# Performance work log

Hardware: AMD Instinct MI355X
Metric: run time of the kernel (lower is better)

The kernel has to match this reference:

```python
import jax, jax.numpy as jnp
import numpy as np
from jax import lax

NBINS = 256


def setup_inputs() -> dict:
    key = jax.random.key(0)
    y_pred = jax.random.uniform(key, (64, 3, 512, 512), dtype=jnp.float32)
    return {"y_pred": y_pred}


def reference(y_pred):
    # Faithful to: per-batch torch.histc(bins=256) (range = data min/max),
    # normalize to probs, entropy in bits with 0*log2(0)=0, mean over batch.
    B = y_pred.shape[0]
    x = y_pred.reshape(B, -1)  # [B, N]
    mn = jnp.min(x, axis=1, keepdims=True)
    mx = jnp.max(x, axis=1, keepdims=True)
    # torch.histc: if min == max they are adjusted to min-1 / max+1
    rng = jnp.where(mx > mn, mx - mn, 2.0)
    lo = jnp.where(mx > mn, mn, mn - 1.0)
    idx = jnp.clip(((x - lo) * (NBINS / rng)).astype(jnp.int32), 0, NBINS - 1)
    idx = lax.stop_gradient(idx)  # binning is non-differentiable (as in torch.histc)
    hist = jax.vmap(lambda i: jnp.bincount(i, length=NBINS))(idx)  # [B, 256]
    hist = hist.astype(y_pred.dtype)
    p = hist / jnp.sum(hist, axis=1, keepdims=True)
    safe_p = jnp.where(p == 0, 1.0, p)  # log2(1)=0 -> contributes 0
    ent = -jnp.sum(p * jnp.log2(safe_p), axis=1)  # [B], entropy in bits
    return jnp.mean(ent)
```

## Files before the change

kernel.cpp:

```cpp
#include <hip/hip_runtime.h>

#define NBINS   256
#define B       64
#define NPB     786432
#define NF4     (NPB / 4)
#define BPB     16
#define THREADS 256

__device__ __forceinline__ unsigned fenc(float f) {
    unsigned u = __float_as_uint(f);
    return (u & 0x80000000u) ? ~u : (u | 0x80000000u);
}
__device__ __forceinline__ float fdec(unsigned u) {
    unsigned v = (u & 0x80000000u) ? (u & 0x7FFFFFFFu) : ~u;
    return __uint_as_float(v);
}

__global__ __launch_bounds__(THREADS) void k_init(unsigned* __restrict__ mm,
                                                  unsigned* __restrict__ hist) {
    int i = blockIdx.x * blockDim.x + threadIdx.x;
    if (i < B) { mm[2 * i] = 0xFFFFFFFFu; mm[2 * i + 1] = 0u; }
    if (i < B * NBINS) hist[i] = 0u;
}

__global__ __launch_bounds__(THREADS) void k_minmax(const float4* __restrict__ x,
                                                    unsigned* __restrict__ mm) {
    const int batch = blockIdx.x / BPB;
    const int blk   = blockIdx.x % BPB;
    const float4* p = x + (long long)batch * NF4;

    float mn = 3.402823466e38f, mx = -3.402823466e38f;
    int t = blk * THREADS + threadIdx.x;
    #pragma unroll 4
    for (int i = t; i < NF4; i += BPB * THREADS) {
        float4 v = p[i];
        mn = fminf(mn, fminf(fminf(v.x, v.y), fminf(v.z, v.w)));
        mx = fmaxf(mx, fmaxf(fmaxf(v.x, v.y), fmaxf(v.z, v.w)));
    }
    for (int o = 32; o > 0; o >>= 1) {
        mn = fminf(mn, __shfl_down(mn, o));
        mx = fmaxf(mx, __shfl_down(mx, o));
    }
    __shared__ float smn[4], smx[4];
    int wid = threadIdx.x >> 6;
    if ((threadIdx.x & 63) == 0) { smn[wid] = mn; smx[wid] = mx; }
    __syncthreads();
    if (threadIdx.x == 0) {
        mn = fminf(fminf(smn[0], smn[1]), fminf(smn[2], smn[3]));
        mx = fmaxf(fmaxf(smx[0], smx[1]), fmaxf(smx[2], smx[3]));
        atomicMin(&mm[2 * batch],     fenc(mn));
        atomicMax(&mm[2 * batch + 1], fenc(mx));
    }
}

__global__ __launch_bounds__(THREADS) void k_hist(const float4* __restrict__ x,
                                                  const unsigned* __restrict__ mm,
                                                  unsigned* __restrict__ hist) {
    const int batch = blockIdx.x / BPB;
    const int blk   = blockIdx.x % BPB;

    __shared__ unsigned lh[4][NBINS];
    for (int i = threadIdx.x; i < 4 * NBINS; i += THREADS)
        ((unsigned*)lh)[i] = 0u;
    __syncthreads();

    const float mn = fdec(mm[2 * batch]);
    const float mx = fdec(mm[2 * batch + 1]);
    const float rng   = (mx > mn) ? (mx - mn) : 2.0f;
    const float lo    = (mx > mn) ? mn : (mn - 1.0f);
    const float scale = (float)NBINS / rng;

    unsigned* h = lh[threadIdx.x >> 6];
    const float4* p = x + (long long)batch * NF4;
    int t = blk * THREADS + threadIdx.x;
    for (int i = t; i < NF4; i += BPB * THREADS) {
        float4 v = p[i];
        int i0 = (int)((v.x - lo) * scale);
        int i1 = (int)((v.y - lo) * scale);
        int i2 = (int)((v.z - lo) * scale);
        int i3 = (int)((v.w - lo) * scale);
        i0 = min(max(i0, 0), NBINS - 1);
        i1 = min(max(i1, 0), NBINS - 1);
        i2 = min(max(i2, 0), NBINS - 1);
        i3 = min(max(i3, 0), NBINS - 1);
        atomicAdd(&h[i0], 1u);
        atomicAdd(&h[i1], 1u);
        atomicAdd(&h[i2], 1u);
        atomicAdd(&h[i3], 1u);
    }
    __syncthreads();

    unsigned* gh = hist + batch * NBINS;
    for (int i = threadIdx.x; i < NBINS; i += THREADS) {
        unsigned s = lh[0][i] + lh[1][i] + lh[2][i] + lh[3][i];
        if (s) atomicAdd(&gh[i], s);
    }
}

__global__ __launch_bounds__(THREADS) void k_entropy(const unsigned* __restrict__ hist,
                                                     float* __restrict__ out) {
    const float invN = 1.0f / (float)NPB;
    float sum = 0.0f;
    for (int b = 0; b < B; ++b) {
        unsigned c = hist[b * NBINS + threadIdx.x];
        if (c) {
            float pv = (float)c * invN;
            sum += pv * log2f(pv);
        }
    }
    for (int o = 32; o > 0; o >>= 1) sum += __shfl_down(sum, o);
    __shared__ float s[4];
    int wid = threadIdx.x >> 6;
    if ((threadIdx.x & 63) == 0) s[wid] = sum;
    __syncthreads();
    if (threadIdx.x == 0)
        out[0] = -(s[0] + s[1] + s[2] + s[3]) / (float)B;
}

extern "C" void kernel_launch(void* const* d_in, const int* in_sizes, int n_in,
                              void* d_out, int out_size, void* d_ws, size_t ws_size,
                              hipStream_t stream) {
    const float* x = (const float*)d_in[0];
    float* out = (float*)d_out;
    unsigned* mm   = (unsigned*)d_ws;
    unsigned* hist = mm + 2 * B;

    hipLaunchKernelGGL(k_init, dim3((B * NBINS + THREADS - 1) / THREADS),
                       dim3(THREADS), 0, stream, mm, hist);
    hipLaunchKernelGGL(k_minmax, dim3(B * BPB), dim3(THREADS), 0, stream,
                       (const float4*)x, mm);
    hipLaunchKernelGGL(k_hist, dim3(B * BPB), dim3(THREADS), 0, stream,
                       (const float4*)x, mm, hist);
    hipLaunchKernelGGL(k_entropy, dim3(1), dim3(THREADS), 0, stream, hist, out);
}
```

Baseline: 302.0 us.

## Fuse min/max, histogram and entropy into one cooperative kernel with grid syncs

Merges the init, min/max, histogram and entropy kernels into a single cooperative launch that uses grid-wide syncs between phases. Each block writes its own partial min/max, and the histogram phase reduces the 16 per-batch partials directly, which removes the encoded float atomics and the separate init kernel. The histogram zeroing is folded into the min/max phase. This saves launch gaps and keeps data possibly warm in cache between passes. It adds grid-sync cost and depends on all 1024 blocks being co-resident, with a fallback to three separate kernels if the cooperative launch fails.

```diff
diff --git a/kernel.cpp b/kernel.cpp
--- a/kernel.cpp
+++ b/kernel.cpp
@@ -1,4 +1,7 @@
 #include <hip/hip_runtime.h>
+#include <hip/hip_cooperative_groups.h>
+
+namespace cg = cooperative_groups;
 
 #define NBINS   256
 #define B       64
@@ -6,28 +9,17 @@
 #define NF4     (NPB / 4)
 #define BPB     16
 #define THREADS 256
+#define GRID    (B * BPB)
 
-__device__ __forceinline__ unsigned fenc(float f) {
-    unsigned u = __float_as_uint(f);
-    return (u & 0x80000000u) ? ~u : (u | 0x80000000u);
-}
-__device__ __forceinline__ float fdec(unsigned u) {
-    unsigned v = (u & 0x80000000u) ? (u & 0x7FFFFFFFu) : ~u;
-    return __uint_as_float(v);
-}
 
-__global__ __launch_bounds__(THREADS) void k_init(unsigned* __restrict__ mm,
-                                                  unsigned* __restrict__ hist) {
-    int i = blockIdx.x * blockDim.x + threadIdx.x;
-    if (i < B) { mm[2 * i] = 0xFFFFFFFFu; mm[2 * i + 1] = 0u; }
-    if (i < B * NBINS) hist[i] = 0u;
-}
+__device__ __forceinline__ void phase_minmax(const float4* __restrict__ x,
+                                             float2* __restrict__ pb,
+                                             unsigned* __restrict__ bhist) {
+    if (blockIdx.x < B) bhist[blockIdx.x * NBINS + threadIdx.x] = 0u;
 
-__global__ __launch_bounds__(THREADS) void k_minmax(const float4* __restrict__ x,
-                                                    unsigned* __restrict__ mm) {
     const int batch = blockIdx.x / BPB;
     const int blk   = blockIdx.x % BPB;
-    const float4* p = x + (long long)batch * NF4;
+    const float4* p = x + (size_t)batch * NF4;
 
     float mn = 3.402823466e38f, mx = -3.402823466e38f;
     int t = blk * THREADS + threadIdx.x;
@@ -48,30 +40,34 @@
     if (threadIdx.x == 0) {
         mn = fminf(fminf(smn[0], smn[1]), fminf(smn[2], smn[3]));
         mx = fmaxf(fmaxf(smx[0], smx[1]), fmaxf(smx[2], smx[3]));
-        atomicMin(&mm[2 * batch],     fenc(mn));
-        atomicMax(&mm[2 * batch + 1], fenc(mx));
+        pb[blockIdx.x] = make_float2(mn, mx);
     }
 }
 
-__global__ __launch_bounds__(THREADS) void k_hist(const float4* __restrict__ x,
-                                                  const unsigned* __restrict__ mm,
-                                                  unsigned* __restrict__ hist) {
+__device__ __forceinline__ void phase_hist(const float4* __restrict__ x,
+                                           const float2* __restrict__ pb,
+                                           unsigned* __restrict__ bhist) {
     const int batch = blockIdx.x / BPB;
     const int blk   = blockIdx.x % BPB;
+
+    float mn = 3.402823466e38f, mx = -3.402823466e38f;
+    #pragma unroll
+    for (int j = 0; j < BPB; ++j) {
+        float2 v = pb[batch * BPB + j];
+        mn = fminf(mn, v.x);
+        mx = fmaxf(mx, v.y);
+    }
+    const float rng   = (mx > mn) ? (mx - mn) : 2.0f;
+    const float lo    = (mx > mn) ? mn : (mn - 1.0f);
+    const float scale = (float)NBINS / rng;
 
     __shared__ unsigned lh[4][NBINS];
     for (int i = threadIdx.x; i < 4 * NBINS; i += THREADS)
         ((unsigned*)lh)[i] = 0u;
     __syncthreads();
 
-    const float mn = fdec(mm[2 * batch]);
-    const float mx = fdec(mm[2 * batch + 1]);
-    const float rng   = (mx > mn) ? (mx - mn) : 2.0f;
-    const float lo    = (mx > mn) ? mn : (mn - 1.0f);
-    const float scale = (float)NBINS / rng;
-
     unsigned* h = lh[threadIdx.x >> 6];
-    const float4* p = x + (long long)batch * NF4;
+    const float4* p = x + (size_t)batch * NF4;
     int t = blk * THREADS + threadIdx.x;
     for (int i = t; i < NF4; i += BPB * THREADS) {
         float4 v = p[i];
@@ -90,19 +86,19 @@
     }
     __syncthreads();
 
-    unsigned* gh = hist + batch * NBINS;
+    unsigned* gh = bhist + batch * NBINS;
     for (int i = threadIdx.x; i < NBINS; i += THREADS) {
         unsigned s = lh[0][i] + lh[1][i] + lh[2][i] + lh[3][i];
         if (s) atomicAdd(&gh[i], s);
     }
 }
 
-__global__ __launch_bounds__(THREADS) void k_entropy(const unsigned* __restrict__ hist,
-                                                     float* __restrict__ out) {
+__device__ __forceinline__ void phase_entropy(const unsigned* __restrict__ bhist,
+                                              float* __restrict__ out) {
     const float invN = 1.0f / (float)NPB;
     float sum = 0.0f;
     for (int b = 0; b < B; ++b) {
-        unsigned c = hist[b * NBINS + threadIdx.x];
+        unsigned c = bhist[b * NBINS + threadIdx.x];
         if (c) {
             float pv = (float)c * invN;
             sum += pv * log2f(pv);
@@ -117,19 +113,58 @@
         out[0] = -(s[0] + s[1] + s[2] + s[3]) / (float)B;
 }
 
+__global__ __launch_bounds__(THREADS, 4) void k_fused(const float4* __restrict__ x,
+                                                      float2* __restrict__ pb,
+                                                      unsigned* __restrict__ bhist,
+                                                      float* __restrict__ out) {
+    cg::grid_group g = cg::this_grid();
+    phase_minmax(x, pb, bhist);
+    g.sync();
+    phase_hist(x, pb, bhist);
+    g.sync();
+    if (blockIdx.x == 0) phase_entropy(bhist, out);
+}
+
+__global__ __launch_bounds__(THREADS) void k_p1(const float4* __restrict__ x,
+                                                float2* __restrict__ pb,
+                                                unsigned* __restrict__ bhist) {
+    phase_minmax(x, pb, bhist);
+}
+__global__ __launch_bounds__(THREADS) void k_p2(const float4* __restrict__ x,
+                                                const float2* __restrict__ pb,
+                                                unsigned* __restrict__ bhist) {
+    phase_hist(x, pb, bhist);
+}
+__global__ __launch_bounds__(THREADS) void k_p3(const unsigned* __restrict__ bhist,
+                                                float* __restrict__ out) {
+    phase_entropy(bhist, out);
+}
+
 extern "C" void kernel_launch(void* const* d_in, const int* in_sizes, int n_in,
                               void* d_out, int out_size, void* d_ws, size_t ws_size,
                               hipStream_t stream) {
-    const float* x = (const float*)d_in[0];
-    float* out = (float*)d_out;
-    unsigned* mm   = (unsigned*)d_ws;
-    unsigned* hist = mm + 2 * B;
+    const float4* x = (const float4*)d_in[0];
+    float* out      = (float*)d_out;
+    float2* pb      = (float2*)d_ws;
+    unsigned* bhist = (unsigned*)((char*)d_ws + GRID * sizeof(float2));
 
-    hipLaunchKernelGGL(k_init, dim3((B * NBINS + THREADS - 1) / THREADS),
-                       dim3(THREADS), 0, stream, mm, hist);
-    hipLaunchKernelGGL(k_minmax, dim3(B * BPB), dim3(THREADS), 0, stream,
-                       (const float4*)x, mm);
-    hipLaunchKernelGGL(k_hist, dim3(B * BPB), dim3(THREADS), 0, stream,
-                       (const float4*)x, mm, hist);
-    hipLaunchKernelGGL(k_entropy, dim3(1), dim3(THREADS), 0, stream, hist, out);
+    static int coop = -1;
+    if (coop < 0) {
+        int v = 0;
+        hipDeviceGetAttribute(&v, hipDeviceAttributeCooperativeLaunch, 0);
+        coop = v;
+    }
+
+    bool launched = false;
+    if (coop) {
+        void* args[] = { (void*)&x, (void*)&pb, (void*)&bhist, (void*)&out };
+        hipError_t err = hipLaunchCooperativeKernel((void*)k_fused, dim3(GRID),
+                                                    dim3(THREADS), args, 0, stream);
+        launched = (err == hipSuccess);
+    }
+    if (!launched) {
+        hipLaunchKernelGGL(k_p1, dim3(GRID), dim3(THREADS), 0, stream, x, pb, bhist);
+        hipLaunchKernelGGL(k_p2, dim3(GRID), dim3(THREADS), 0, stream, x, pb, bhist);
+        hipLaunchKernelGGL(k_p3, dim3(1), dim3(THREADS), 0, stream, bhist, out);
+    }
 }
```

Measured after the change: 533.8 us. +76.8%, slower.

## Drop init kernel, write per-block min/max partials, double blocks per batch

Applied to the files above, without the earlier changes.

Removes the separate init kernel by zeroing the histogram inside the min/max kernel. Global atomic min/max with float encoding is replaced by per-block partial writes, which the histogram kernel reduces itself. Blocks per batch go from 16 to 32, so more workgroups share the two memory-bound passes. The cost is that every histogram block redundantly reads all partials for its batch, and there are twice as many global histogram atomic merges.

```diff
diff --git a/kernel.cpp b/kernel.cpp
--- a/kernel.cpp
+++ b/kernel.cpp
@@ -4,30 +4,19 @@
 #define B       64
 #define NPB     786432
 #define NF4     (NPB / 4)
-#define BPB     16
+#define BPB     32
 #define THREADS 256
+#define GRID    (B * BPB)
 
-__device__ __forceinline__ unsigned fenc(float f) {
-    unsigned u = __float_as_uint(f);
-    return (u & 0x80000000u) ? ~u : (u | 0x80000000u);
-}
-__device__ __forceinline__ float fdec(unsigned u) {
-    unsigned v = (u & 0x80000000u) ? (u & 0x7FFFFFFFu) : ~u;
-    return __uint_as_float(v);
-}
-
-__global__ __launch_bounds__(THREADS) void k_init(unsigned* __restrict__ mm,
-                                                  unsigned* __restrict__ hist) {
-    int i = blockIdx.x * blockDim.x + threadIdx.x;
-    if (i < B) { mm[2 * i] = 0xFFFFFFFFu; mm[2 * i + 1] = 0u; }
-    if (i < B * NBINS) hist[i] = 0u;
-}
 
 __global__ __launch_bounds__(THREADS) void k_minmax(const float4* __restrict__ x,
-                                                    unsigned* __restrict__ mm) {
+                                                    float2* __restrict__ pb,
+                                                    unsigned* __restrict__ hist) {
+    if (blockIdx.x < B) hist[blockIdx.x * NBINS + threadIdx.x] = 0u;
+
     const int batch = blockIdx.x / BPB;
     const int blk   = blockIdx.x % BPB;
-    const float4* p = x + (long long)batch * NF4;
+    const float4* p = x + (size_t)batch * NF4;
 
     float mn = 3.402823466e38f, mx = -3.402823466e38f;
     int t = blk * THREADS + threadIdx.x;
@@ -48,30 +37,34 @@
     if (threadIdx.x == 0) {
         mn = fminf(fminf(smn[0], smn[1]), fminf(smn[2], smn[3]));
         mx = fmaxf(fmaxf(smx[0], smx[1]), fmaxf(smx[2], smx[3]));
-        atomicMin(&mm[2 * batch],     fenc(mn));
-        atomicMax(&mm[2 * batch + 1], fenc(mx));
+        pb[blockIdx.x] = make_float2(mn, mx);
     }
 }
 
 __global__ __launch_bounds__(THREADS) void k_hist(const float4* __restrict__ x,
-                                                  const unsigned* __restrict__ mm,
+                                                  const float2* __restrict__ pb,
                                                   unsigned* __restrict__ hist) {
     const int batch = blockIdx.x / BPB;
     const int blk   = blockIdx.x % BPB;
+
+    float mn = 3.402823466e38f, mx = -3.402823466e38f;
+    #pragma unroll
+    for (int j = 0; j < BPB; ++j) {
+        float2 v = pb[batch * BPB + j];
+        mn = fminf(mn, v.x);
+        mx = fmaxf(mx, v.y);
+    }
+    const float rng   = (mx > mn) ? (mx - mn) : 2.0f;
+    const float lo    = (mx > mn) ? mn : (mn - 1.0f);
+    const float scale = (float)NBINS / rng;
 
     __shared__ unsigned lh[4][NBINS];
     for (int i = threadIdx.x; i < 4 * NBINS; i += THREADS)
         ((unsigned*)lh)[i] = 0u;
     __syncthreads();
 
-    const float mn = fdec(mm[2 * batch]);
-    const float mx = fdec(mm[2 * batch + 1]);
-    const float rng   = (mx > mn) ? (mx - mn) : 2.0f;
-    const float lo    = (mx > mn) ? mn : (mn - 1.0f);
-    const float scale = (float)NBINS / rng;
-
     unsigned* h = lh[threadIdx.x >> 6];
-    const float4* p = x + (long long)batch * NF4;
+    const float4* p = x + (size_t)batch * NF4;
     int t = blk * THREADS + threadIdx.x;
     for (int i = t; i < NF4; i += BPB * THREADS) {
         float4 v = p[i];
@@ -101,6 +94,7 @@
                                                      float* __restrict__ out) {
     const float invN = 1.0f / (float)NPB;
     float sum = 0.0f;
+    #pragma unroll 8
     for (int b = 0; b < B; ++b) {
         unsigned c = hist[b * NBINS + threadIdx.x];
         if (c) {
@@ -120,16 +114,15 @@
 extern "C" void kernel_launch(void* const* d_in, const int* in_sizes, int n_in,
                               void* d_out, int out_size, void* d_ws, size_t ws_size,
                               hipStream_t stream) {
-    const float* x = (const float*)d_in[0];
-    float* out = (float*)d_out;
-    unsigned* mm   = (unsigned*)d_ws;
-    unsigned* hist = mm + 2 * B;
+    const float4* x = (const float4*)d_in[0];
+    float* out      = (float*)d_out;
+    float2* pb      = (float2*)d_ws;
+    unsigned* hist  = (unsigned*)((char*)d_ws + GRID * sizeof(float2));
 
-    hipLaunchKernelGGL(k_init, dim3((B * NBINS + THREADS - 1) / THREADS),
-                       dim3(THREADS), 0, stream, mm, hist);
-    hipLaunchKernelGGL(k_minmax, dim3(B * BPB), dim3(THREADS), 0, stream,
-                       (const float4*)x, mm);
-    hipLaunchKernelGGL(k_hist, dim3(B * BPB), dim3(THREADS), 0, stream,
-                       (const float4*)x, mm, hist);
-    hipLaunchKernelGGL(k_entropy, dim3(1), dim3(THREADS), 0, stream, hist, out);
+    hipLaunchKernelGGL(k_minmax, dim3(GRID), dim3(THREADS), 0, stream,
+                       x, pb, hist);
+    hipLaunchKernelGGL(k_hist, dim3(GRID), dim3(THREADS), 0, stream,
+                       x, pb, hist);
+    hipLaunchKernelGGL(k_entropy, dim3(1), dim3(THREADS), 0, stream,
+                       hist, out);
 }
```

After: 307.2 us. Within noise of the previous version (+1.7%).
